# Optimization experiments

Measured on AMD Instinct MI355X. Metric: run time of the kernel, lower is better.

Reference implementation:

```python
import jax, jax.numpy as jnp
import numpy as np
from jax import lax

DIM = 180
NUM_HEADS = 6
WS = 16                     # window_size
OWS = 24                    # overlap_win_size = int(16 * 1.5)
PAD = (OWS - WS) // 2       # 4
EPS = 1e-5


def setup_inputs() -> dict:
    key = jax.random.key(0)
    ks = jax.random.split(key, 4)
    B, H, W, C = 1, 256, 256, DIM
    x = jax.random.normal(ks[0], (B, H * W, C), dtype=jnp.float32)
    s = 0.05  # keep logits in a sane range
    return {
        "x": x,
        "norm_w": jnp.ones((C,), jnp.float32),
        "norm_b": jnp.zeros((C,), jnp.float32),
        "q_w": jax.random.normal(ks[1], (C, C), jnp.float32) * s,
        "q_b": jnp.zeros((C,), jnp.float32),
        "kv_w": jax.random.normal(ks[2], (C, 2 * C), jnp.float32) * s,
        "kv_b": jnp.zeros((2 * C,), jnp.float32),
        "proj_w": jax.random.normal(ks[3], (C, C), jnp.float32) * s,
        "proj_b": jnp.zeros((C,), jnp.float32),
        "H": H,
        "W": W,
    }


def _ocab(x, norm_w, norm_b, q_w, q_b, kv_w, kv_b, proj_w, proj_b, H, W):
    B, N, C = x.shape
    nh, hd = NUM_HEADS, C // NUM_HEADS
    scale = hd ** (-0.5)
    nHw, nWw = H // WS, W // WS
    nW = nHw * nWw

    shortcut = x
    # LayerNorm
    mu = jnp.mean(x, axis=-1, keepdims=True)
    var = jnp.var(x, axis=-1, keepdims=True)
    xn = (x - mu) * lax.rsqrt(var + EPS) * norm_w + norm_b

    feat = xn.reshape(B, H, W, C)

    # --- query: non-overlapping window partition -> [B*nW, WS*WS, C]
    qw = feat.reshape(B, nHw, WS, nWw, WS, C).transpose(0, 1, 3, 2, 4, 5)
    qw = qw.reshape(B * nW, WS * WS, C)
    q = qw @ q_w + q_b

    # --- key/value: overlapping windows via unfold (kernel=OWS, stride=WS, pad=PAD)
    feat_chw = feat.transpose(0, 3, 1, 2)  # [B, C, H, W]
    patches = lax.conv_general_dilated_patches(
        feat_chw, filter_shape=(OWS, OWS), window_strides=(WS, WS),
        padding=((PAD, PAD), (PAD, PAD)))  # [B, C*OWS*OWS, nHw, nWw], channel-major
    kv_feat = patches.reshape(B, C, OWS * OWS, nW).transpose(0, 3, 2, 1)
    kv_feat = kv_feat.reshape(B * nW, OWS * OWS, C)
    kv = kv_feat @ kv_w + kv_b
    k, v = jnp.split(kv, 2, axis=-1)

    # --- multi-head attention: 256 queries vs 576 keys per window
    q = q.reshape(B * nW, WS * WS, nh, hd).transpose(0, 2, 1, 3)
    k = k.reshape(B * nW, OWS * OWS, nh, hd).transpose(0, 2, 1, 3)
    v = v.reshape(B * nW, OWS * OWS, nh, hd).transpose(0, 2, 1, 3)

    attn = jnp.einsum('whqd,whkd->whqk', q, k) * scale
    attn = jax.nn.softmax(attn, axis=-1)
    out = jnp.einsum('whqk,whkd->whqd', attn, v)
    out = out.transpose(0, 2, 1, 3).reshape(B * nW, WS * WS, C)
    out = out @ proj_w + proj_b

    # --- window reverse + residual
    out = out.reshape(B, nHw, nWw, WS, WS, C).transpose(0, 1, 3, 2, 4, 5)
    out = out.reshape(B, N, C)
    return shortcut + out


def reference(x, norm_w, norm_b, q_w, q_b, kv_w, kv_b, proj_w, proj_b, H, W):
    return _ocab(x, norm_w, norm_b, q_w, q_b, kv_w, kv_b, proj_w, proj_b, H, W)
```

## Files before the change

kernel.cpp:

```cpp
#include <hip/hip_runtime.h>
#include <math.h>

typedef __bf16 bf16x8 __attribute__((ext_vector_type(8)));
typedef float f32x4 __attribute__((ext_vector_type(4)));
typedef unsigned short ushort_t;

static __device__ __forceinline__ unsigned short f2bf(float f) {
  union { float f; unsigned int u; } c; c.f = f;
  unsigned int u = c.u;
  unsigned int r = u + 0x7FFFu + ((u >> 16) & 1u);
  return (unsigned short)(r >> 16);
}

#define CDIM 180
#define CPAD 192
#define NTOK 65536

#define SCL2E 0.26339361f

static __device__ __forceinline__ unsigned pk_bf(float a, float b) {
  union { float f; unsigned u; } ca, cb; ca.f = a; cb.f = b;
  return __builtin_amdgcn_perm(cb.u, ca.u, 0x07060302u);
}

__global__ __launch_bounds__(256) void prep_k(
    const float* __restrict__ q_w, const float* __restrict__ q_b,
    const float* __restrict__ kv_w, const float* __restrict__ kv_b,
    const float* __restrict__ p_w, const float* __restrict__ p_b,
    ushort_t* __restrict__ wqkvt, ushort_t* __restrict__ pwt,
    float* __restrict__ qkvb, float* __restrict__ pbp,
    ushort_t* __restrict__ k_bias_row, ushort_t* __restrict__ vt4_bias_grp)
{
  int i = blockIdx.x * 256 + threadIdx.x;
  if (i < 110592) {
    int n = i / 192, k = i % 192;
    float v = 0.f;
    if (k < CDIM) {
      if (n < 192) { int h = n >> 5, d = n & 31; if (d < 30) v = q_w[k * CDIM + h * 30 + d] * SCL2E; }
      else { int cn = n - 192; int part = cn >= 192; int c2 = cn - part * 192;
             int h = c2 >> 5, d = c2 & 31;
             if (d < 30) v = kv_w[k * 360 + part * 180 + h * 30 + d]; }
    }
    wqkvt[i] = f2bf(v);
    return;
  }
  i -= 110592;
  if (i < 36864) {
    int n = i / 192, r = i % 192, h = r >> 5, d = r & 31;
    float v = (d < 30 && n < CDIM) ? p_w[(h * 30 + d) * CDIM + n] : 0.f;
    pwt[i] = f2bf(v);
    return;
  }
  i -= 36864;
  if (i < 576) {
    float v = 0.f;
    if (i < 192) { int h = i >> 5, d = i & 31; if (d < 30) v = q_b[h * 30 + d] * SCL2E; }
    else { int cn = i - 192; int part = cn >= 192; int c2 = cn - part * 192;
           int h = c2 >> 5, d = c2 & 31;
           if (d < 30) v = kv_b[part * 180 + h * 30 + d];
           else if (part == 1 && d == 30) v = 1.0f; }
    qkvb[i] = v;
    return;
  }
  i -= 576;
  if (i < 192) { pbp[i] = (i < CDIM) ? p_b[i] : 0.f; return; }
  i -= 192;
  if (i < 192) {
    int h = i >> 5, d = i & 31;
    k_bias_row[i] = (d < 30) ? f2bf(kv_b[h * 30 + d]) : (ushort_t)0;
    return;
  }
  i -= 192;
  if (i < 768) {
    int d = i >> 2, h = d >> 5, dd = d & 31;
    float v = 0.f;
    if (dd < 30) v = kv_b[180 + h * 30 + dd];
    else if (dd == 30) v = 1.0f;
    vt4_bias_grp[i] = f2bf(v);
    return;
  }
}

__global__ __launch_bounds__(256) void ln_k(const float* __restrict__ x,
    const float* __restrict__ nw, const float* __restrict__ nb,
    ushort_t* __restrict__ xn)
{
  const int lane = threadIdx.x & 63, wave = threadIdx.x >> 6;
  const int row = blockIdx.x * 4 + wave;
  const float* xr = x + (size_t)row * CDIM;
  float f0 = xr[lane];
  float f1 = xr[lane + 64];
  float f2 = (lane < 52) ? xr[lane + 128] : 0.f;
  float sum = f0 + f1 + f2;
  float sq = f0 * f0 + f1 * f1 + f2 * f2;
  #pragma unroll
  for (int off = 1; off < 64; off <<= 1) {
    sum += __shfl_xor(sum, off, 64);
    sq  += __shfl_xor(sq, off, 64);
  }
  const float inv_n = 1.0f / 180.0f;
  float mean = sum * inv_n;
  float var = sq * inv_n - mean * mean;
  float rs = rsqrtf(var + 1e-5f);
  ushort_t* xo = xn + (size_t)row * CPAD;
  #pragma unroll
  for (int e = 0; e < 3; ++e) {
    int col = lane + e * 64;
    float v = 0.f;
    if (col < CDIM) v = (( (e==0)?f0 : (e==1)?f1 : f2 ) - mean) * rs * nw[col] + nb[col];
    xo[col] = f2bf(v);
  }
}

template<int MODE>
__global__ __launch_bounds__(256) void gemm_k(const ushort_t* __restrict__ A,
    const ushort_t* __restrict__ Wt, const float* __restrict__ bias,
    ushort_t* __restrict__ q_out, ushort_t* __restrict__ k_out,
    ushort_t* __restrict__ vt_out,
    float* __restrict__ outf, const float* __restrict__ resid)
{
  constexpr int NT = (MODE == 0) ? 9 : 3;
  __shared__ __align__(16) ushort_t aS[128 * 200];
  const int tid = threadIdx.x;
  const int lane = tid & 63, wave = tid >> 6;
  const int quad = lane >> 4, l16 = lane & 15;
  const int wm = wave & 1, wn = wave >> 1;
  const int bm = blockIdx.x;

  {
    const ushort_t* Ab = A + (size_t)bm * 128 * 192;
    #pragma unroll
    for (int it = 0; it < 12; ++it) {
      int f = it * 256 + tid;
      int row = f / 24, kq = f % 24;
      uint4 v = *reinterpret_cast<const uint4*>(Ab + row * 192 + kq * 8);
      *reinterpret_cast<uint4*>(&aS[row * 200 + kq * 8]) = v;
    }
  }
  __syncthreads();

  for (int nt0 = 0; nt0 < NT; ++nt0) {
    f32x4 acc[4][2] = {};
    #pragma unroll
    for (int ks = 0; ks < 6; ++ks) {
      bf16x8 af[4], bfr[2];
      #pragma unroll
      for (int nt = 0; nt < 2; ++nt) {
        int n = nt0 * 64 + wn * 32 + nt * 16 + l16;
        bfr[nt] = *reinterpret_cast<const bf16x8*>(Wt + (size_t)n * 192 + ks * 32 + quad * 8);
      }
      #pragma unroll
      for (int mt = 0; mt < 4; ++mt)
        af[mt] = *reinterpret_cast<const bf16x8*>(&aS[(wm * 64 + mt * 16 + l16) * 200 + ks * 32 + quad * 8]);
      #pragma unroll
      for (int mt = 0; mt < 4; ++mt)
        #pragma unroll
        for (int nt = 0; nt < 2; ++nt)
          acc[mt][nt] = __builtin_amdgcn_mfma_f32_16x16x32_bf16(af[mt], bfr[nt], acc[mt][nt], 0, 0, 0);
    }
    #pragma unroll
    for (int mt = 0; mt < 4; ++mt) {
      int row = bm * 128 + wm * 64 + mt * 16 + quad * 4;
      #pragma unroll
      for (int nt = 0; nt < 2; ++nt) {
        int ncol = nt0 * 64 + wn * 32 + nt * 16 + l16;
        float bv = bias[ncol];
        if (MODE == 0 && nt0 >= 6) {
          int d = ncol - 384;
          unsigned p0 = pk_bf(acc[mt][nt][0] + bv, acc[mt][nt][1] + bv);
          unsigned p1 = pk_bf(acc[mt][nt][2] + bv, acc[mt][nt][3] + bv);
          uint2 val; val.x = p0; val.y = p1;
          *reinterpret_cast<uint2*>(vt_out + (size_t)row * 192 + d * 4) = val;
        } else {
          #pragma unroll
          for (int r = 0; r < 4; ++r) {
            int rr = row + r;
            float v = acc[mt][nt][r] + bv;
            if (MODE == 0) {
              if (ncol < 192) q_out[(size_t)rr * CPAD + ncol] = f2bf(v);
              else k_out[(size_t)rr * CPAD + (ncol - 192)] = f2bf(v);
            } else {
              if (ncol < CDIM) outf[(size_t)rr * CDIM + ncol] = v + resid[(size_t)rr * CDIM + ncol];
            }
          }
        }
      }
    }
  }
}

__global__ __launch_bounds__(256, 4) void attn_k(const ushort_t* __restrict__ q_tok,
    const ushort_t* __restrict__ k_tok, const ushort_t* __restrict__ vt4,
    ushort_t* __restrict__ ao)
{
  const int w = blockIdx.x, h = blockIdx.y;
  const int tid = threadIdx.x;
  const int lane = tid & 63, wave = tid >> 6;
  const int quad = lane >> 4, l16 = lane & 15;
  const int wy = w >> 4, wx = w & 15;
  const int tok0 = wy * 16 * 256 + wx * 16;
  const int hc = h * 32;
  const int ybase = wy * 16 - 4, xbase = wx * 16 - 4;

  bf16x8 qf[4];
  #pragma unroll
  for (int qt = 0; qt < 4; ++qt) {
    int qi = wave * 64 + qt * 16 + l16;
    int token = tok0 + (qi >> 4) * 256 + (qi & 15);
    qf[qt] = *reinterpret_cast<const bf16x8*>(q_tok + (size_t)token * CPAD + hc + quad * 8);
  }

  const int key0 = ((l16 >> 2) << 3) + (l16 & 3);

  int kpy[3][2], ktx[3][2]; bool kxin[3][2];
  int vpy[3][2], vtx[3][2]; bool vxin[3][2];
  #pragma unroll
  for (int cm = 0; cm < 3; ++cm) {
    #pragma unroll
    for (int j = 0; j < 2; ++j) {
      int pk = 32 * cm + key0 + 4 * j;
      int py = pk / 24, px = pk - py * 24;
      kpy[cm][j] = py; ktx[cm][j] = xbase + px;
      kxin[cm][j] = (unsigned)(xbase + px) < 256u;
      int pv = 32 * cm + quad * 8 + 4 * j;
      int pyv = pv / 24, pxv = pv - pyv * 24;
      vpy[cm][j] = pyv; vtx[cm][j] = xbase + pxv;
      vxin[cm][j] = (unsigned)(xbase + pxv) < 256u;
    }
  }
  const int dOff0 = (hc + l16) * 4, dOff1 = (hc + 16 + l16) * 4;

  auto loadK = [&](int c, bf16x8* kf) {
    const int cm = c % 3, c3 = c / 3;
    const int yrow = ybase + 4 * c3;
    #pragma unroll
    for (int kt = 0; kt < 2; ++kt) {
      int y = yrow + kpy[cm][kt];
      bool inb = kxin[cm][kt] && ((unsigned)y < 256u);
      int t = inb ? (y * 256 + ktx[cm][kt]) : NTOK;
      kf[kt] = *reinterpret_cast<const bf16x8*>(k_tok + (size_t)t * CPAD + hc + quad * 8);
    }
  };
  auto loadV = [&](int c, uint2* va, uint2* vb) {
    const int cm = c % 3, c3 = c / 3;
    const int yrow = ybase + 4 * c3;
    #pragma unroll
    for (int h2 = 0; h2 < 2; ++h2) {
      int y = yrow + vpy[cm][h2];
      bool inb = vxin[cm][h2] && ((unsigned)y < 256u);
      int t = inb ? (y * 256 + vtx[cm][h2]) : NTOK;
      const ushort_t* gp = vt4 + (size_t)t * 192;
      va[h2] = *reinterpret_cast<const uint2*>(gp + dOff0);
      vb[h2] = *reinterpret_cast<const uint2*>(gp + dOff1);
    }
  };

  f32x4 o[4][2] = {};
  f32x4 zero = {0.f, 0.f, 0.f, 0.f};

  bf16x8 kbuf[2][2];
  uint2 vabuf[2][2], vbbuf[2][2];

  loadK(0, kbuf[0]);
  loadV(0, vabuf[0], vbbuf[0]);

  #pragma unroll
  for (int c = 0; c < 18; ++c) {
    const int cur = c & 1, nxt = cur ^ 1;
    if (c < 17) {
      loadK(c + 1, kbuf[nxt]);
      loadV(c + 1, vabuf[nxt], vbbuf[nxt]);
    }

    bf16x8 vf0, vf1;
    {
      union { unsigned u[4]; bf16x8 v; } a_;
      a_.u[0] = vabuf[cur][0].x; a_.u[1] = vabuf[cur][0].y;
      a_.u[2] = vabuf[cur][1].x; a_.u[3] = vabuf[cur][1].y;
      vf0 = a_.v;
      a_.u[0] = vbbuf[cur][0].x; a_.u[1] = vbbuf[cur][0].y;
      a_.u[2] = vbbuf[cur][1].x; a_.u[3] = vbbuf[cur][1].y;
      vf1 = a_.v;
    }

    __builtin_amdgcn_s_setprio(1);
    #pragma unroll
    for (int qt = 0; qt < 4; ++qt) {
      f32x4 s0 = __builtin_amdgcn_mfma_f32_16x16x32_bf16(kbuf[cur][0], qf[qt], zero, 0, 0, 0);
      f32x4 s1 = __builtin_amdgcn_mfma_f32_16x16x32_bf16(kbuf[cur][1], qf[qt], zero, 0, 0, 0);
      union { unsigned u[4]; bf16x8 v; } pk;
      pk.u[0] = pk_bf(__builtin_amdgcn_exp2f(s0[0]), __builtin_amdgcn_exp2f(s0[1]));
      pk.u[1] = pk_bf(__builtin_amdgcn_exp2f(s0[2]), __builtin_amdgcn_exp2f(s0[3]));
      pk.u[2] = pk_bf(__builtin_amdgcn_exp2f(s1[0]), __builtin_amdgcn_exp2f(s1[1]));
      pk.u[3] = pk_bf(__builtin_amdgcn_exp2f(s1[2]), __builtin_amdgcn_exp2f(s1[3]));
      o[qt][0] = __builtin_amdgcn_mfma_f32_16x16x32_bf16(pk.v, vf0, o[qt][0], 0, 0, 0);
      o[qt][1] = __builtin_amdgcn_mfma_f32_16x16x32_bf16(pk.v, vf1, o[qt][1], 0, 0, 0);
    }
    __builtin_amdgcn_s_setprio(0);
  }

  #pragma unroll
  for (int qt = 0; qt < 4; ++qt) {
    #pragma unroll
    for (int r = 0; r < 4; ++r) {
      float l = __shfl(o[qt][1][r], (lane & 48) + 14, 64);
      float inv = 1.0f / l;
      int qi = wave * 64 + qt * 16 + quad * 4 + r;
      int token = tok0 + (qi >> 4) * 256 + (qi & 15);
      ao[(size_t)token * CPAD + hc + l16]      = f2bf(o[qt][0][r] * inv);
      ao[(size_t)token * CPAD + hc + 16 + l16] = f2bf(o[qt][1][r] * inv);
    }
  }
}

extern "C" void kernel_launch(void* const* d_in, const int* in_sizes, int n_in,
                              void* d_out, int out_size, void* d_ws, size_t ws_size,
                              hipStream_t stream) {
  const float* x      = (const float*)d_in[0];
  const float* norm_w = (const float*)d_in[1];
  const float* norm_b = (const float*)d_in[2];
  const float* q_w    = (const float*)d_in[3];
  const float* q_b    = (const float*)d_in[4];
  const float* kv_w   = (const float*)d_in[5];
  const float* kv_b   = (const float*)d_in[6];
  const float* p_w    = (const float*)d_in[7];
  const float* p_b    = (const float*)d_in[8];

  char* base = (char*)d_ws;
  size_t off = 0;
  auto alloc = [&](size_t bytes) { char* p = base + off; off = (off + bytes + 255) & ~(size_t)255; return p; };
  ushort_t* xn_p  = (ushort_t*)alloc((size_t)NTOK * CPAD * 2);
  ushort_t* q_tok = (ushort_t*)alloc((size_t)NTOK * CPAD * 2);
  ushort_t* k_tok = (ushort_t*)alloc((size_t)(NTOK + 1) * CPAD * 2);
  ushort_t* vt4   = (ushort_t*)alloc((size_t)(NTOK + 4) * 192 * 2);
  ushort_t* wqkvt = (ushort_t*)alloc(576 * 192 * 2);
  ushort_t* pwt   = (ushort_t*)alloc(192 * 192 * 2);
  float* qkvb = (float*)alloc(576 * 4);
  float* pbp  = (float*)alloc(192 * 4);
  ushort_t* ao = xn_p;

  prep_k<<<583, 256, 0, stream>>>(q_w, q_b, kv_w, kv_b, p_w, p_b,
                                  wqkvt, pwt, qkvb, pbp,
                                  k_tok + (size_t)NTOK * CPAD,
                                  vt4 + (size_t)NTOK * 192);
  ln_k<<<NTOK / 4, 256, 0, stream>>>(x, norm_w, norm_b, xn_p);
  gemm_k<0><<<NTOK / 128, 256, 0, stream>>>(xn_p, wqkvt, qkvb, q_tok, k_tok, vt4, nullptr, nullptr);
  attn_k<<<dim3(256, 6), 256, 0, stream>>>(q_tok, k_tok, vt4, ao);
  gemm_k<1><<<NTOK / 128, 256, 0, stream>>>(ao, pwt, pbp, nullptr, nullptr, nullptr, (float*)d_out, x);
}
```

Measured before the change: 233.6 us.

## Split K/V chunk loads across waves and share them through LDS

Before this change, every wave in the attention kernel loaded the full K and V fragments for each chunk straight from global memory, so the same data was fetched four times per block. Now each wave loads one quarter (two waves take the K tiles, two take the V halves) and writes it to a double-buffered shared-memory tile. All waves read that tile from LDS, with a block barrier after each chunk. This cuts redundant global/L2 traffic but adds LDS writes and reads plus 18 __syncthreads per block, which may stall waves that previously ran independently.

```diff
diff --git a/kernel.cpp b/kernel.cpp
--- a/kernel.cpp
+++ b/kernel.cpp
@@ -202,6 +202,8 @@
   const int hc = h * 32;
   const int ybase = wy * 16 - 4, xbase = wx * 16 - 4;
 
+  __shared__ __align__(16) ushort_t kvS[2][4][512];
+
   bf16x8 qf[4];
   #pragma unroll
   for (int qt = 0; qt < 4; ++qt) {
@@ -230,64 +232,61 @@
   }
   const int dOff0 = (hc + l16) * 4, dOff1 = (hc + 16 + l16) * 4;
 
-  auto loadK = [&](int c, bf16x8* kf) {
+  bf16x8 kreg;
+  uint2 v0reg, v1reg;
+  auto load_role = [&](int c) {
     const int cm = c % 3, c3 = c / 3;
     const int yrow = ybase + 4 * c3;
-    #pragma unroll
-    for (int kt = 0; kt < 2; ++kt) {
+    if (wave == 0 || wave == 3) {
+      const int kt = (wave == 0) ? 0 : 1;
       int y = yrow + kpy[cm][kt];
       bool inb = kxin[cm][kt] && ((unsigned)y < 256u);
       int t = inb ? (y * 256 + ktx[cm][kt]) : NTOK;
-      kf[kt] = *reinterpret_cast<const bf16x8*>(k_tok + (size_t)t * CPAD + hc + quad * 8);
-    }
-  };
-  auto loadV = [&](int c, uint2* va, uint2* vb) {
-    const int cm = c % 3, c3 = c / 3;
-    const int yrow = ybase + 4 * c3;
-    #pragma unroll
-    for (int h2 = 0; h2 < 2; ++h2) {
+      kreg = *reinterpret_cast<const bf16x8*>(k_tok + (size_t)t * CPAD + hc + quad * 8);
+    } else {
+      const int h2 = wave - 1;
       int y = yrow + vpy[cm][h2];
       bool inb = vxin[cm][h2] && ((unsigned)y < 256u);
       int t = inb ? (y * 256 + vtx[cm][h2]) : NTOK;
       const ushort_t* gp = vt4 + (size_t)t * 192;
-      va[h2] = *reinterpret_cast<const uint2*>(gp + dOff0);
-      vb[h2] = *reinterpret_cast<const uint2*>(gp + dOff1);
+      v0reg = *reinterpret_cast<const uint2*>(gp + dOff0);
+      v1reg = *reinterpret_cast<const uint2*>(gp + dOff1);
+    }
+  };
+  auto write_role = [&](int b) {
+    if (wave == 0)      *reinterpret_cast<bf16x8*>(&kvS[b][0][lane * 8]) = kreg;
+    else if (wave == 3) *reinterpret_cast<bf16x8*>(&kvS[b][1][lane * 8]) = kreg;
+    else if (wave == 1) {
+      *reinterpret_cast<uint2*>(&kvS[b][2][lane * 8])     = v0reg;
+      *reinterpret_cast<uint2*>(&kvS[b][3][lane * 8])     = v1reg;
+    } else {
+      *reinterpret_cast<uint2*>(&kvS[b][2][lane * 8 + 4]) = v0reg;
+      *reinterpret_cast<uint2*>(&kvS[b][3][lane * 8 + 4]) = v1reg;
     }
   };
 
   f32x4 o[4][2] = {};
   f32x4 zero = {0.f, 0.f, 0.f, 0.f};
 
-  bf16x8 kbuf[2][2];
-  uint2 vabuf[2][2], vbbuf[2][2];
-
-  loadK(0, kbuf[0]);
-  loadV(0, vabuf[0], vbbuf[0]);
+  load_role(0);
+  write_role(0);
+  __syncthreads();
 
   #pragma unroll
   for (int c = 0; c < 18; ++c) {
-    const int cur = c & 1, nxt = cur ^ 1;
-    if (c < 17) {
-      loadK(c + 1, kbuf[nxt]);
-      loadV(c + 1, vabuf[nxt], vbbuf[nxt]);
-    }
-
-    bf16x8 vf0, vf1;
-    {
-      union { unsigned u[4]; bf16x8 v; } a_;
-      a_.u[0] = vabuf[cur][0].x; a_.u[1] = vabuf[cur][0].y;
-      a_.u[2] = vabuf[cur][1].x; a_.u[3] = vabuf[cur][1].y;
-      vf0 = a_.v;
-      a_.u[0] = vbbuf[cur][0].x; a_.u[1] = vbbuf[cur][0].y;
-      a_.u[2] = vbbuf[cur][1].x; a_.u[3] = vbbuf[cur][1].y;
-      vf1 = a_.v;
-    }
+    const int b = c & 1;
+    if (c < 17) load_role(c + 1);
+
+    bf16x8 kf0 = *reinterpret_cast<const bf16x8*>(&kvS[b][0][lane * 8]);
+    bf16x8 kf1 = *reinterpret_cast<const bf16x8*>(&kvS[b][1][lane * 8]);
+    bf16x8 vf0 = *reinterpret_cast<const bf16x8*>(&kvS[b][2][lane * 8]);
+    bf16x8 vf1 = *reinterpret_cast<const bf16x8*>(&kvS[b][3][lane * 8]);
 
     __builtin_amdgcn_s_setprio(1);
     #pragma unroll
     for (int qt = 0; qt < 4; ++qt) {
-      f32x4 s0 = __builtin_amdgcn_mfma_f32_16x16x32_bf16(kbuf[cur][0], qf[qt], zero, 0, 0, 0);
-      f32x4 s1 = __builtin_amdgcn_mfma_f32_16x16x32_bf16(kbuf[cur][1], qf[qt], zero, 0, 0, 0);
+      f32x4 s0 = __builtin_amdgcn_mfma_f32_16x16x32_bf16(kf0, qf[qt], zero, 0, 0, 0);
+      f32x4 s1 = __builtin_amdgcn_mfma_f32_16x16x32_bf16(kf1, qf[qt], zero, 0, 0, 0);
       union { unsigned u[4]; bf16x8 v; } pk;
       pk.u[0] = pk_bf(__builtin_amdgcn_exp2f(s0[0]), __builtin_amdgcn_exp2f(s0[1]));
       pk.u[1] = pk_bf(__builtin_amdgcn_exp2f(s0[2]), __builtin_amdgcn_exp2f(s0[3]));
@@ -297,6 +296,11 @@
       o[qt][1] = __builtin_amdgcn_mfma_f32_16x16x32_bf16(pk.v, vf1, o[qt][1], 0, 0, 0);
     }
     __builtin_amdgcn_s_setprio(0);
+
+    if (c < 17) {
+      write_role(b ^ 1);
+      __syncthreads();
+    }
   }
 
   #pragma unroll
```

Measured after the change: 236.6 us. Within noise of the previous version (+1.3%).

## Add interior-window fast path with precomputed offsets and deeper K/V prefetch

Applied to the files above, without the earlier changes.

Attention windows that lie fully inside the image now take a specialised path. It drops the bounds checks and per-iteration token index math, using precomputed 32-bit byte offsets plus a constant row stride. This path also switches from double to triple buffering of K/V register loads, so two chunks are in flight ahead of compute to hide global load latency. Border windows keep the old masked double-buffered path. The cost is more code size and more live registers, which may lower occupancy.

```diff
diff --git a/kernel.cpp b/kernel.cpp
--- a/kernel.cpp
+++ b/kernel.cpp
@@ -212,82 +212,23 @@
 
   const int key0 = ((l16 >> 2) << 3) + (l16 & 3);
 
-  int kpy[3][2], ktx[3][2]; bool kxin[3][2];
-  int vpy[3][2], vtx[3][2]; bool vxin[3][2];
-  #pragma unroll
-  for (int cm = 0; cm < 3; ++cm) {
-    #pragma unroll
-    for (int j = 0; j < 2; ++j) {
-      int pk = 32 * cm + key0 + 4 * j;
-      int py = pk / 24, px = pk - py * 24;
-      kpy[cm][j] = py; ktx[cm][j] = xbase + px;
-      kxin[cm][j] = (unsigned)(xbase + px) < 256u;
-      int pv = 32 * cm + quad * 8 + 4 * j;
-      int pyv = pv / 24, pxv = pv - pyv * 24;
-      vpy[cm][j] = pyv; vtx[cm][j] = xbase + pxv;
-      vxin[cm][j] = (unsigned)(xbase + pxv) < 256u;
-    }
-  }
-  const int dOff0 = (hc + l16) * 4, dOff1 = (hc + 16 + l16) * 4;
-
-  auto loadK = [&](int c, bf16x8* kf) {
-    const int cm = c % 3, c3 = c / 3;
-    const int yrow = ybase + 4 * c3;
-    #pragma unroll
-    for (int kt = 0; kt < 2; ++kt) {
-      int y = yrow + kpy[cm][kt];
-      bool inb = kxin[cm][kt] && ((unsigned)y < 256u);
-      int t = inb ? (y * 256 + ktx[cm][kt]) : NTOK;
-      kf[kt] = *reinterpret_cast<const bf16x8*>(k_tok + (size_t)t * CPAD + hc + quad * 8);
-    }
-  };
-  auto loadV = [&](int c, uint2* va, uint2* vb) {
-    const int cm = c % 3, c3 = c / 3;
-    const int yrow = ybase + 4 * c3;
-    #pragma unroll
-    for (int h2 = 0; h2 < 2; ++h2) {
-      int y = yrow + vpy[cm][h2];
-      bool inb = vxin[cm][h2] && ((unsigned)y < 256u);
-      int t = inb ? (y * 256 + vtx[cm][h2]) : NTOK;
-      const ushort_t* gp = vt4 + (size_t)t * 192;
-      va[h2] = *reinterpret_cast<const uint2*>(gp + dOff0);
-      vb[h2] = *reinterpret_cast<const uint2*>(gp + dOff1);
-    }
-  };
-
   f32x4 o[4][2] = {};
   f32x4 zero = {0.f, 0.f, 0.f, 0.f};
 
-  bf16x8 kbuf[2][2];
-  uint2 vabuf[2][2], vbbuf[2][2];
-
-  loadK(0, kbuf[0]);
-  loadV(0, vabuf[0], vbbuf[0]);
-
-  #pragma unroll
-  for (int c = 0; c < 18; ++c) {
-    const int cur = c & 1, nxt = cur ^ 1;
-    if (c < 17) {
-      loadK(c + 1, kbuf[nxt]);
-      loadV(c + 1, vabuf[nxt], vbbuf[nxt]);
-    }
-
+  auto compute = [&](const bf16x8* kf, const uint2* va, const uint2* vb) {
     bf16x8 vf0, vf1;
     {
       union { unsigned u[4]; bf16x8 v; } a_;
-      a_.u[0] = vabuf[cur][0].x; a_.u[1] = vabuf[cur][0].y;
-      a_.u[2] = vabuf[cur][1].x; a_.u[3] = vabuf[cur][1].y;
+      a_.u[0] = va[0].x; a_.u[1] = va[0].y; a_.u[2] = va[1].x; a_.u[3] = va[1].y;
       vf0 = a_.v;
-      a_.u[0] = vbbuf[cur][0].x; a_.u[1] = vbbuf[cur][0].y;
-      a_.u[2] = vbbuf[cur][1].x; a_.u[3] = vbbuf[cur][1].y;
+      a_.u[0] = vb[0].x; a_.u[1] = vb[0].y; a_.u[2] = vb[1].x; a_.u[3] = vb[1].y;
       vf1 = a_.v;
     }
-
     __builtin_amdgcn_s_setprio(1);
     #pragma unroll
     for (int qt = 0; qt < 4; ++qt) {
-      f32x4 s0 = __builtin_amdgcn_mfma_f32_16x16x32_bf16(kbuf[cur][0], qf[qt], zero, 0, 0, 0);
-      f32x4 s1 = __builtin_amdgcn_mfma_f32_16x16x32_bf16(kbuf[cur][1], qf[qt], zero, 0, 0, 0);
+      f32x4 s0 = __builtin_amdgcn_mfma_f32_16x16x32_bf16(kf[0], qf[qt], zero, 0, 0, 0);
+      f32x4 s1 = __builtin_amdgcn_mfma_f32_16x16x32_bf16(kf[1], qf[qt], zero, 0, 0, 0);
       union { unsigned u[4]; bf16x8 v; } pk;
       pk.u[0] = pk_bf(__builtin_amdgcn_exp2f(s0[0]), __builtin_amdgcn_exp2f(s0[1]));
       pk.u[1] = pk_bf(__builtin_amdgcn_exp2f(s0[2]), __builtin_amdgcn_exp2f(s0[3]));
@@ -297,6 +238,100 @@
       o[qt][1] = __builtin_amdgcn_mfma_f32_16x16x32_bf16(pk.v, vf1, o[qt][1], 0, 0, 0);
     }
     __builtin_amdgcn_s_setprio(0);
+  };
+
+  const bool interior = ((unsigned)(wy - 1) < 14u) && ((unsigned)(wx - 1) < 14u);
+
+  if (interior) {
+    unsigned koff[3][2], voff[3][2];
+    #pragma unroll
+    for (int cm = 0; cm < 3; ++cm) {
+      #pragma unroll
+      for (int j = 0; j < 2; ++j) {
+        int pk = 32 * cm + key0 + 4 * j;
+        int py = pk / 24, px = pk - py * 24;
+        koff[cm][j] = (unsigned)((((ybase + py) * 256 + xbase + px) * 384) + (hc + quad * 8) * 2);
+        int pv = 32 * cm + quad * 8 + 4 * j;
+        int pyv = pv / 24, pxv = pv - pyv * 24;
+        voff[cm][j] = (unsigned)((((ybase + pyv) * 256 + xbase + pxv) * 384) + (hc + l16) * 8);
+      }
+    }
+    const char* kp = (const char*)k_tok;
+    const char* vp = (const char*)vt4;
+    auto lK = [&](int c, bf16x8* kf) {
+      const int cm = c % 3; const unsigned cb = (unsigned)(c / 3) * 393216u;
+      #pragma unroll
+      for (int kt = 0; kt < 2; ++kt)
+        kf[kt] = *reinterpret_cast<const bf16x8*>(kp + (size_t)(koff[cm][kt] + cb));
+    };
+    auto lV = [&](int c, uint2* va, uint2* vb) {
+      const int cm = c % 3; const unsigned cb = (unsigned)(c / 3) * 393216u;
+      #pragma unroll
+      for (int h2 = 0; h2 < 2; ++h2) {
+        const char* g = vp + (size_t)(voff[cm][h2] + cb);
+        va[h2] = *reinterpret_cast<const uint2*>(g);
+        vb[h2] = *reinterpret_cast<const uint2*>(g + 128);
+      }
+    };
+    bf16x8 kbuf[3][2]; uint2 vabuf[3][2], vbbuf[3][2];
+    lK(0, kbuf[0]); lV(0, vabuf[0], vbbuf[0]);
+    lK(1, kbuf[1]); lV(1, vabuf[1], vbbuf[1]);
+    #pragma unroll
+    for (int c = 0; c < 18; ++c) {
+      const int cur = c % 3, nxt = (c + 2) % 3;
+      if (c < 16) { lK(c + 2, kbuf[nxt]); lV(c + 2, vabuf[nxt], vbbuf[nxt]); }
+      compute(kbuf[cur], vabuf[cur], vbbuf[cur]);
+    }
+  } else {
+    int kpy[3][2], ktx[3][2]; bool kxin[3][2];
+    int vpy[3][2], vtx[3][2]; bool vxin[3][2];
+    #pragma unroll
+    for (int cm = 0; cm < 3; ++cm) {
+      #pragma unroll
+      for (int j = 0; j < 2; ++j) {
+        int pk = 32 * cm + key0 + 4 * j;
+        int py = pk / 24, px = pk - py * 24;
+        kpy[cm][j] = py; ktx[cm][j] = xbase + px;
+        kxin[cm][j] = (unsigned)(xbase + px) < 256u;
+        int pv = 32 * cm + quad * 8 + 4 * j;
+        int pyv = pv / 24, pxv = pv - pyv * 24;
+        vpy[cm][j] = pyv; vtx[cm][j] = xbase + pxv;
+        vxin[cm][j] = (unsigned)(xbase + pxv) < 256u;
+      }
+    }
+    const int dOff0 = (hc + l16) * 4, dOff1 = (hc + 16 + l16) * 4;
+    auto loadK = [&](int c, bf16x8* kf) {
+      const int cm = c % 3, c3 = c / 3;
+      const int yrow = ybase + 4 * c3;
+      #pragma unroll
+      for (int kt = 0; kt < 2; ++kt) {
+        int y = yrow + kpy[cm][kt];
+        bool inb = kxin[cm][kt] && ((unsigned)y < 256u);
+        int t = inb ? (y * 256 + ktx[cm][kt]) : NTOK;
+        kf[kt] = *reinterpret_cast<const bf16x8*>(k_tok + (size_t)t * CPAD + hc + quad * 8);
+      }
+    };
+    auto loadV = [&](int c, uint2* va, uint2* vb) {
+      const int cm = c % 3, c3 = c / 3;
+      const int yrow = ybase + 4 * c3;
+      #pragma unroll
+      for (int h2 = 0; h2 < 2; ++h2) {
+        int y = yrow + vpy[cm][h2];
+        bool inb = vxin[cm][h2] && ((unsigned)y < 256u);
+        int t = inb ? (y * 256 + vtx[cm][h2]) : NTOK;
+        const ushort_t* gp = vt4 + (size_t)t * 192;
+        va[h2] = *reinterpret_cast<const uint2*>(gp + dOff0);
+        vb[h2] = *reinterpret_cast<const uint2*>(gp + dOff1);
+      }
+    };
+    bf16x8 kbuf[2][2]; uint2 vabuf[2][2], vbbuf[2][2];
+    loadK(0, kbuf[0]); loadV(0, vabuf[0], vbbuf[0]);
+    #pragma unroll
+    for (int c = 0; c < 18; ++c) {
+      const int cur = c & 1, nxt = cur ^ 1;
+      if (c < 17) { loadK(c + 1, kbuf[nxt]); loadV(c + 1, vabuf[nxt], vbbuf[nxt]); }
+      compute(kbuf[cur], vabuf[cur], vbbuf[cur]);
+    }
   }
 
   #pragma unroll
```

New measurement: 235.1 us. No clear change (+0.6%).
